# Performance work log

Hardware: AMD Instinct MI355X
Metric: run time of the kernel (lower is better)

The kernel has to match this reference:

```python
import jax, jax.numpy as jnp
import numpy as np

N_NODES = 100000
N_EDGES = 1600000
NFEAT, NHID, NCLASS = 256, 128, 40


def gcn_layer(x, W, b, src, dst, dinv):
    # GCNConv (Kipf): D^-1/2 (A + I) D^-1/2 (X W) + b
    h = x @ W                                    # [N, out]
    coef = (dinv[src] * dinv[dst])[:, None]      # [E, 1] sym-norm per edge
    msg = h[src] * coef                          # gather (irregular access)
    agg = jax.ops.segment_sum(msg, dst, num_segments=N_NODES)
    agg = agg + h * (dinv * dinv)[:, None]       # self-loop contribution
    return agg + b


def setup_inputs() -> dict:
    key = jax.random.key(0)
    ks = jax.random.split(key, 8)
    x = jax.random.normal(ks[0], (N_NODES, NFEAT), dtype=jnp.float32)
    edge_index = jax.random.randint(ks[1], (2, N_EDGES), 0, N_NODES, dtype=jnp.int32)
    def glorot(k, fi, fo):
        s = (6.0 / (fi + fo)) ** 0.5
        return jax.random.uniform(k, (fi, fo), jnp.float32, -s, s)
    return {
        "x": x,
        "edge_index": edge_index,
        "W1": glorot(ks[2], NFEAT, NHID), "b1": jnp.zeros((NHID,), jnp.float32),
        "W2": glorot(ks[3], NHID, NHID), "b2": jnp.zeros((NHID,), jnp.float32),
        "W3": glorot(ks[4], NHID, NCLASS), "b3": jnp.zeros((NCLASS,), jnp.float32),
    }


def reference(x, edge_index, W1, b1, W2, b2, W3, b3):
    src, dst = edge_index[0], edge_index[1]
    # degree with self-loops (count incoming edges per node + 1)
    deg = jax.ops.segment_sum(jnp.ones((N_EDGES,), jnp.float32), dst,
                              num_segments=N_NODES) + 1.0
    dinv = jax.lax.rsqrt(deg)
    h = jax.nn.relu(gcn_layer(x, W1, b1, src, dst, dinv))
    # dropout is identity at eval time
    h = jax.nn.relu(gcn_layer(h, W2, b2, src, dst, dinv))
    h = gcn_layer(h, W3, b3, src, dst, dinv)
    return jax.nn.log_softmax(h, axis=1)
```

## Files before the change

kernel.cpp:

```cpp
#include <hip/hip_runtime.h>
#include <math.h>

#define NFEAT 256
#define NHID 128
#define NCLASS 40
#define BNODES 128
#define BSHIFT 7
#define BCAP 2688
#define MAXBK 1024
#define EPB 16384

typedef unsigned short ushort_t;
typedef unsigned int uint_t;
typedef unsigned char uchar_t;
typedef __attribute__((ext_vector_type(8))) short bf16x8;
typedef __attribute__((ext_vector_type(4))) float f32x4;
typedef __attribute__((ext_vector_type(2))) float f32x2;

static __device__ inline float bf2f(ushort_t u) {
    union { uint_t u; float f; } v; v.u = (uint_t)u << 16; return v.f;
}
static __device__ inline float lo2f(uint_t u) {
    union { uint_t u; float f; } v; v.u = u << 16; return v.f;
}
static __device__ inline float hi2f(uint_t u) {
    union { uint_t u; float f; } v; v.u = u & 0xFFFF0000u; return v.f;
}
static __device__ inline ushort_t f2bf(float f) {
    uint_t u = __float_as_uint(f);
    u += 0x7FFF + ((u >> 16) & 1);
    return (ushort_t)(u >> 16);
}
static __device__ inline float dot2bf(uint_t pk, uint_t mask, float c) {
    float r;
    asm("v_dot2_f32_bf16 %0, %1, %2, %3" : "=v"(r) : "v"(pk), "v"(mask), "v"(c));
    return r;
}
#define LOMASK 0x00003F80u
#define HIMASK 0x3F800000u

static __device__ __forceinline__ void gload16(const void* g, void* l) {
    __builtin_amdgcn_global_load_lds(
        (const __attribute__((address_space(1))) uint_t*)g,
        (__attribute__((address_space(3))) uint_t*)l, 16, 0, 0);
}

static __device__ inline ushort_t pk2fp8(float a, float b) {
    return (ushort_t)__builtin_amdgcn_cvt_pk_fp8_f32(a, b, 0, false);
}
static __device__ inline f32x2 unpk_lo(uint_t w) {
    return __builtin_amdgcn_cvt_pk_f32_fp8(w, false);
}
static __device__ inline f32x2 unpk_hi(uint_t w) {
    return __builtin_amdgcn_cvt_pk_f32_fp8(w, true);
}


__global__ __launch_bounds__(256) void k_ehist(const int* __restrict__ dst,
                                               int* __restrict__ cnt,
                                               int E, int nbk, int nblk) {
    __shared__ int hist[MAXBK];
    int tid = threadIdx.x, be = blockIdx.x;
    for (int i = tid; i < nbk; i += 256) hist[i] = 0;
    __syncthreads();
    int e0 = be * EPB, e1 = min(e0 + EPB, E);
    for (int e = e0 + tid; e < e1; e += 256)
        atomicAdd(&hist[dst[e] >> BSHIFT], 1);
    __syncthreads();
    for (int i = tid; i < nbk; i += 256)
        cnt[(size_t)i * nblk + be] = hist[i];
}

__global__ __launch_bounds__(128) void k_escan(int* __restrict__ cnt,
                                               int* __restrict__ bcnt, int nblk) {
    __shared__ int buf[128];
    int b = blockIdx.x, tid = threadIdx.x;
    int v = (tid < nblk) ? cnt[(size_t)b * nblk + tid] : 0;
    buf[tid] = v;
    __syncthreads();
    for (int off = 1; off < 128; off <<= 1) {
        int t = (tid >= off) ? buf[tid - off] : 0;
        __syncthreads();
        buf[tid] += t;
        __syncthreads();
    }
    if (tid < nblk) cnt[(size_t)b * nblk + tid] = buf[tid] - v;
    if (tid == 127) bcnt[b] = buf[127];
}

__global__ __launch_bounds__(256) void k_escatter(const int* __restrict__ src,
                                                  const int* __restrict__ dst,
                                                  const int* __restrict__ cnt,
                                                  uint_t* __restrict__ bstore,
                                                  int E, int nbk, int nblk) {
    __shared__ int cur[MAXBK];
    int tid = threadIdx.x, be = blockIdx.x;
    for (int i = tid; i < nbk; i += 256)
        cur[i] = cnt[(size_t)i * nblk + be];
    __syncthreads();
    int e0 = be * EPB, e1 = min(e0 + EPB, E);
    for (int e = e0 + tid; e < e1; e += 256) {
        int d = dst[e];
        int b = d >> BSHIFT;
        int p = atomicAdd(&cur[b], 1);
        if (p < BCAP)
            bstore[(size_t)b * BCAP + p] = ((uint_t)(d & (BNODES - 1)) << 20) | (uint_t)src[e];
    }
}


__global__ __launch_bounds__(256) void k_bsort(const uint_t* __restrict__ bstore,
                                               const int* __restrict__ bcnt,
                                               uint_t* __restrict__ colsort,
                                               int* __restrict__ rp,
                                               float* __restrict__ dinv, int N) {
    __shared__ uint_t rec[BCAP];
    __shared__ uint_t srt[BCAP];
    __shared__ int hist[BNODES];
    __shared__ int scan[BNODES];
    __shared__ int cur[BNODES];
    int b = blockIdx.x, tid = threadIdx.x;
    if (tid < BNODES) hist[tid] = 0;
    __syncthreads();
    int cnt = min(bcnt[b], BCAP);
    const uint_t* gp = &bstore[(size_t)b * BCAP];
    for (int e = tid; e < cnt; e += 256) {
        uint_t r = gp[e];
        rec[e] = r;
        atomicAdd(&hist[r >> 20], 1);
    }
    __syncthreads();
    if (tid < BNODES) scan[tid] = hist[tid];
    __syncthreads();
    for (int off = 1; off < BNODES; off <<= 1) {
        int v = 0;
        if (tid < BNODES && tid >= off) v = scan[tid - off];
        __syncthreads();
        if (tid < BNODES) scan[tid] += v;
        __syncthreads();
    }
    if (tid < BNODES) cur[tid] = scan[tid] - hist[tid];
    __syncthreads();
    for (int e = tid; e < cnt; e += 256) {
        uint_t r = rec[e];
        int p = atomicAdd(&cur[r >> 20], 1);
        srt[p] = r & 0xFFFFF;
    }
    __syncthreads();
    uint_t* cs = &colsort[(size_t)b * BCAP];
    for (int e = tid; e < cnt; e += 256) cs[e] = srt[e];
    if (tid < BNODES) {
        rp[b * (BNODES + 1) + tid] = scan[tid] - hist[tid];
        int n = b * BNODES + tid;
        if (n < N) dinv[n] = rsqrtf((float)hist[tid] + 1.0f);
    }
    if (tid == 0) rp[b * (BNODES + 1) + BNODES] = cnt;
}


__global__ __launch_bounds__(256) void k_wtall(const float* __restrict__ W1,
                                               const float* __restrict__ W2,
                                               const float* __restrict__ W3,
                                               ushort_t* __restrict__ T1,
                                               ushort_t* __restrict__ T2,
                                               ushort_t* __restrict__ T3) {
    int idx = blockIdx.x * 256 + threadIdx.x;
    if (idx < NHID * NFEAT) {
        int nrow = idx >> 8, k = idx & 255;
        T1[idx] = f2bf(W1[(size_t)k * NHID + nrow]);
    } else if ((idx -= NHID * NFEAT) < NHID * NHID) {
        int nrow = idx >> 7, kp = idx & 127;
        int s = kp >> 5, pl = kp & 31;
        int k = s * 32 + ((pl & 1) << 4) + (pl >> 1);
        T2[idx] = f2bf(W2[(size_t)k * NHID + nrow]);
    } else if ((idx -= NHID * NHID) < 64 * NHID) {
        int nrow = idx >> 7, kp = idx & 127;
        int s = kp >> 5, pl = kp & 31;
        int k = s * 32 + ((pl & 1) << 4) + (pl >> 1);
        T3[idx] = f2bf(nrow < NCLASS ? W3[(size_t)k * NCLASS + nrow] : 0.f);
    }
}


template<int K, bool A_FP32, int BN, int OST, int MODE>
__global__ __launch_bounds__(512) void k_gemm_mfma(const void* __restrict__ Ap,
                                                   const ushort_t* __restrict__ Whi,
                                                   const float* __restrict__ dinv,
                                                   void* __restrict__ Cv, int n) {
    const int BM = 128, BK = 64;
    __shared__ ushort_t As[BM * BK];
    __shared__ ushort_t Bh[BN * BK];
    const int tid = threadIdx.x;
    const int w = tid >> 6, l = tid & 63;
    const int row0 = blockIdx.x * BM;
    const int NJ = BN / 16;
    f32x4 acc[NJ] = {};

    for (int k0 = 0; k0 < K; k0 += BK) {
        if (A_FP32) {
            int r = tid >> 2;
            if (row0 + r < n) {
                const float* A = (const float*)Ap;
                const float* ap = &A[(size_t)(row0 + r) * K + k0];
#pragma unroll
                for (int h = 0; h < 2; h++) {
                    int q = (tid & 3) * 2 + h;
                    float4 v0 = *(const float4*)&ap[q * 8];
                    float4 v1 = *(const float4*)&ap[q * 8 + 4];
                    ushort4 o0, o1;
                    o0.x = f2bf(v0.x); o0.y = f2bf(v0.y); o0.z = f2bf(v0.z); o0.w = f2bf(v0.w);
                    o1.x = f2bf(v1.x); o1.y = f2bf(v1.y); o1.z = f2bf(v1.z); o1.w = f2bf(v1.w);
                    int pc = q ^ (r & 7);
                    *(ushort4*)&As[r * 64 + pc * 8]     = o0;
                    *(ushort4*)&As[r * 64 + pc * 8 + 4] = o1;
                }
            }
        } else {
            const ushort_t* A = (const ushort_t*)Ap;
#pragma unroll
            for (int m = 0; m < 2; m++) {
                int unit = m * 512 + tid;
                int r = unit >> 3, pc = unit & 7;
                int lc = pc ^ (r & 7);
                int kk = k0 + lc * 8;
                size_t rowg = (size_t)min(row0 + r, n - 1);
                const ushort_t* srcp = &A[(size_t)(kk >> 6) * n * 64 + rowg * 64 + (kk & 63)];
                gload16(srcp, &As[(size_t)unit * 8]);
            }
        }
#pragma unroll
        for (int m = 0; m < BN / 64; m++) {
            int unit = m * 512 + tid;
            int r = unit >> 3, pc = unit & 7;
            int lc = pc ^ (r & 7);
            gload16(&Whi[(size_t)r * K + k0 + lc * 8], &Bh[(size_t)unit * 8]);
        }
        __syncthreads();

        const int lo4 = l & 15;
        const int swz = l & 7;
#pragma unroll
        for (int kh = 0; kh < BK; kh += 32) {
            int q = (kh >> 3) + (l >> 4);
            int ra = w * 16 + lo4;
            bf16x8 a = *(const bf16x8*)&As[ra * 64 + (q ^ swz) * 8];
#pragma unroll
            for (int j = 0; j < NJ; j++) {
                int rb = j * 16 + lo4;
                bf16x8 bh = *(const bf16x8*)&Bh[rb * 64 + (q ^ swz) * 8];
                acc[j] = __builtin_amdgcn_mfma_f32_16x16x32_bf16(a, bh, acc[j], 0, 0, 0);
            }
        }
        __syncthreads();
    }

    float dnv[4];
#pragma unroll
    for (int r = 0; r < 4; r++) {
        int row = row0 + w * 16 + (l >> 4) * 4 + r;
        dnv[r] = (row < n) ? dinv[row] : 0.f;
    }
    const int cb = l & 15;
    if (MODE == 0) {
        uchar_t* C8 = (uchar_t*)Cv;
#pragma unroll
        for (int s = 0; s < NJ / 2; s++) {
            int t = s >> 1, sub = s & 1;
#pragma unroll
            for (int r = 0; r < 4; r++) {
                int row = row0 + w * 16 + (l >> 4) * 4 + r;
                if (row < n) {
                    ushort_t pk = pk2fp8(dnv[r] * acc[2 * s][r], dnv[r] * acc[2 * s + 1][r]);
                    *(ushort_t*)&C8[(size_t)t * n * 64 + (size_t)row * 64 + sub * 32 + cb * 2] = pk;
                }
            }
        }
    } else {
        ushort_t* C = (ushort_t*)Cv;
#pragma unroll
        for (int j = 0; j < NJ; j++) {
#pragma unroll
            for (int r = 0; r < 4; r++) {
                int row = row0 + w * 16 + (l >> 4) * 4 + r;
                if (row < n)
                    C[(size_t)row * OST + j * 16 + cb] = f2bf(dnv[r] * acc[j][r]);
            }
        }
    }
}


__global__ __launch_bounds__(256) void k_agg_slice(const uint_t* __restrict__ colsort,
                                                   const int* __restrict__ rp,
                                                   const uchar_t* __restrict__ h8,
                                                   const float* __restrict__ dinv,
                                                   const float* __restrict__ bias,
                                                   ushort_t* __restrict__ out, int N) {
    __shared__ int srp[BNODES + 1];
    __shared__ uint_t cols[BCAP];
    int blk = blockIdx.x;
    int slice = blk & 1, b = blk >> 1;
    int tid = threadIdx.x;
    if (tid <= BNODES) srp[tid] = rp[b * (BNODES + 1) + tid];
    __syncthreads();
    int cnt = srp[BNODES];
    for (int e = tid; e < cnt; e += 256) cols[e] = colsort[(size_t)b * BCAP + e];
    __syncthreads();
    int fq = tid & 3;
    int q  = tid >> 2;
    const uchar_t* hs = &h8[(size_t)slice * N * 64 + fq * 16];
    float bv[16];
#pragma unroll
    for (int i = 0; i < 16; i++) {
        int p = fq * 16 + i;
        int s = 2 * slice + (p >> 5), pl = p & 31;
        bv[i] = bias[s * 32 + ((pl & 1) << 4) + (pl >> 1)];
    }
    for (int nl = q; nl < BNODES; nl += 64) {
        int n = b * BNODES + nl;
        if (n >= N) break;
        int e = srp[nl], e1 = srp[nl + 1];
        f32x2 a2[8];
        {
            uint4 sv = *(const uint4*)&hs[(size_t)n * 64];
            a2[0] = unpk_lo(sv.x); a2[1] = unpk_hi(sv.x);
            a2[2] = unpk_lo(sv.y); a2[3] = unpk_hi(sv.y);
            a2[4] = unpk_lo(sv.z); a2[5] = unpk_hi(sv.z);
            a2[6] = unpk_lo(sv.w); a2[7] = unpk_hi(sv.w);
        }
        for (; e + 4 <= e1; e += 4) {
            uint4 v[4];
#pragma unroll
            for (int i = 0; i < 4; i++) v[i] = *(const uint4*)&hs[(size_t)cols[e + i] * 64];
#pragma unroll
            for (int i = 0; i < 4; i++) {
                a2[0] += unpk_lo(v[i].x); a2[1] += unpk_hi(v[i].x);
                a2[2] += unpk_lo(v[i].y); a2[3] += unpk_hi(v[i].y);
                a2[4] += unpk_lo(v[i].z); a2[5] += unpk_hi(v[i].z);
                a2[6] += unpk_lo(v[i].w); a2[7] += unpk_hi(v[i].w);
            }
        }
        for (; e < e1; e++) {
            uint4 v = *(const uint4*)&hs[(size_t)cols[e] * 64];
            a2[0] += unpk_lo(v.x); a2[1] += unpk_hi(v.x);
            a2[2] += unpk_lo(v.y); a2[3] += unpk_hi(v.y);
            a2[4] += unpk_lo(v.z); a2[5] += unpk_hi(v.z);
            a2[6] += unpk_lo(v.w); a2[7] += unpk_hi(v.w);
        }
        float dn = dinv[n];
        uint_t o[8];
#pragma unroll
        for (int k = 0; k < 8; k++) {
            float r0 = fmaxf(fmaf(dn, a2[k].x, bv[2 * k]),     0.f);
            float r1 = fmaxf(fmaf(dn, a2[k].y, bv[2 * k + 1]), 0.f);
            o[k] = ((uint_t)f2bf(r1) << 16) | f2bf(r0);
        }
        ushort_t* op = &out[((size_t)slice * N + n) * 64 + fq * 16];
        *(uint4*)&op[0] = make_uint4(o[0], o[1], o[2], o[3]);
        *(uint4*)&op[8] = make_uint4(o[4], o[5], o[6], o[7]);
    }
}


__global__ __launch_bounds__(256) void k_agg40_lsm(const uint_t* __restrict__ colsort,
                                                   const int* __restrict__ rp,
                                                   const ushort_t* __restrict__ h3,
                                                   const float* __restrict__ dinv,
                                                   const float* __restrict__ bias,
                                                   float* __restrict__ out, int N) {
    __shared__ int srp[BNODES + 1];
    __shared__ uint_t cols[BCAP];
    int b = blockIdx.x, tid = threadIdx.x;
    if (tid <= BNODES) srp[tid] = rp[b * (BNODES + 1) + tid];
    __syncthreads();
    int cnt = srp[BNODES];
    for (int e = tid; e < cnt; e += 256) cols[e] = colsort[(size_t)b * BCAP + e];
    __syncthreads();
    int fo = tid & 7;
    int g  = tid >> 3;
    bool act = fo < 5;
    float bv[8];
#pragma unroll
    for (int j = 0; j < 8; j++) bv[j] = act ? bias[fo * 8 + j] : 0.f;
    for (int nl = g; nl < BNODES; nl += 32) {
        int n = b * BNODES + nl;
        if (n >= N) break;
        int e = srp[nl], e1 = srp[nl + 1];
        float a[8] = {0.f, 0.f, 0.f, 0.f, 0.f, 0.f, 0.f, 0.f};
        if (act) {
            uint4 sv = *(const uint4*)&h3[(size_t)n * 64 + fo * 8];
            a[0] = lo2f(sv.x); a[1] = hi2f(sv.x); a[2] = lo2f(sv.y); a[3] = hi2f(sv.y);
            a[4] = lo2f(sv.z); a[5] = hi2f(sv.z); a[6] = lo2f(sv.w); a[7] = hi2f(sv.w);
        }
        for (; e + 4 <= e1; e += 4) {
            if (act) {
                uint4 v[4];
#pragma unroll
                for (int i = 0; i < 4; i++) v[i] = *(const uint4*)&h3[(size_t)cols[e + i] * 64 + fo * 8];
#pragma unroll
                for (int i = 0; i < 4; i++) {
                    a[0] = dot2bf(v[i].x, LOMASK, a[0]); a[1] = dot2bf(v[i].x, HIMASK, a[1]);
                    a[2] = dot2bf(v[i].y, LOMASK, a[2]); a[3] = dot2bf(v[i].y, HIMASK, a[3]);
                    a[4] = dot2bf(v[i].z, LOMASK, a[4]); a[5] = dot2bf(v[i].z, HIMASK, a[5]);
                    a[6] = dot2bf(v[i].w, LOMASK, a[6]); a[7] = dot2bf(v[i].w, HIMASK, a[7]);
                }
            }
        }
        for (; e < e1; e++) {
            if (act) {
                uint4 v = *(const uint4*)&h3[(size_t)cols[e] * 64 + fo * 8];
                a[0] = dot2bf(v.x, LOMASK, a[0]); a[1] = dot2bf(v.x, HIMASK, a[1]);
                a[2] = dot2bf(v.y, LOMASK, a[2]); a[3] = dot2bf(v.y, HIMASK, a[3]);
                a[4] = dot2bf(v.z, LOMASK, a[4]); a[5] = dot2bf(v.z, HIMASK, a[5]);
                a[6] = dot2bf(v.w, LOMASK, a[6]); a[7] = dot2bf(v.w, HIMASK, a[7]);
            }
        }
        float dn = dinv[n];
        float z[8];
        float m = -INFINITY;
#pragma unroll
        for (int j = 0; j < 8; j++) {
            z[j] = act ? fmaf(dn, a[j], bv[j]) : -INFINITY;
            m = fmaxf(m, z[j]);
        }
#pragma unroll
        for (int off = 4; off; off >>= 1) m = fmaxf(m, __shfl_xor(m, off, 8));
        float p = 0.f;
        if (act) {
#pragma unroll
            for (int j = 0; j < 8; j++) p += expf(z[j] - m);
        }
#pragma unroll
        for (int off = 4; off; off >>= 1) p += __shfl_xor(p, off, 8);
        float lse = m + logf(p);
        if (act) {
            float4 o0 = make_float4(z[0] - lse, z[1] - lse, z[2] - lse, z[3] - lse);
            float4 o1 = make_float4(z[4] - lse, z[5] - lse, z[6] - lse, z[7] - lse);
            *(float4*)&out[(size_t)n * NCLASS + fo * 8]     = o0;
            *(float4*)&out[(size_t)n * NCLASS + fo * 8 + 4] = o1;
        }
    }
}


extern "C" void kernel_launch(void* const* d_in, const int* in_sizes, int n_in,
                              void* d_out, int out_size, void* d_ws, size_t ws_size,
                              hipStream_t stream) {
    const float* x  = (const float*)d_in[0];
    const int*   ei = (const int*)d_in[1];
    const float* W1 = (const float*)d_in[2];
    const float* b1 = (const float*)d_in[3];
    const float* W2 = (const float*)d_in[4];
    const float* b2 = (const float*)d_in[5];
    const float* W3 = (const float*)d_in[6];
    const float* b3 = (const float*)d_in[7];
    float* out = (float*)d_out;
    const int N = in_sizes[0] / NFEAT;
    const int E = in_sizes[1] / 2;
    const int* src = ei;
    const int* dst = ei + E;
    const int NBK = (N + BNODES - 1) / BNODES;
    const int NBLK_E = (E + EPB - 1) / EPB;

    char* ws = (char*)d_ws;
    size_t off = 0;
    auto alloc = [&](size_t bytes) -> void* {
        void* p = ws + off;
        off += (bytes + 255) & ~(size_t)255;
        return p;
    };
    int*      bcnt    = (int*)alloc((size_t)NBK * 4);
    int*      ecnt    = (int*)alloc((size_t)NBK * NBLK_E * 4);
    uint_t*   bstore  = (uint_t*)alloc((size_t)NBK * BCAP * 4);
    uint_t*   colsort = (uint_t*)alloc((size_t)NBK * BCAP * 4);
    int*      rp      = (int*)alloc((size_t)NBK * (BNODES + 1) * 4);
    float*    dinv    = (float*)alloc((size_t)N * 4);
    uchar_t*  h8      = (uchar_t*)alloc((size_t)N * NHID);
    ushort_t* abuf    = (ushort_t*)alloc((size_t)N * NHID * 2);
    ushort_t* h3      = (ushort_t*)alloc((size_t)N * 64 * 2);
    ushort_t* Whi1    = (ushort_t*)alloc((size_t)NHID * NFEAT * 2);
    ushort_t* Whi2    = (ushort_t*)alloc((size_t)NHID * NHID * 2);
    ushort_t* Whi3    = (ushort_t*)alloc((size_t)64 * NHID * 2);
    (void)ws_size; (void)n_in; (void)out_size;

    int wtelems = NHID * NFEAT + NHID * NHID + 64 * NHID;
    k_wtall<<<(wtelems + 255) / 256, 256, 0, stream>>>(W1, W2, W3, Whi1, Whi2, Whi3);

    k_ehist<<<NBLK_E, 256, 0, stream>>>(dst, ecnt, E, NBK, NBLK_E);
    k_escan<<<NBK, 128, 0, stream>>>(ecnt, bcnt, NBLK_E);
    k_escatter<<<NBLK_E, 256, 0, stream>>>(src, dst, ecnt, bstore, E, NBK, NBLK_E);
    k_bsort<<<NBK, 256, 0, stream>>>(bstore, bcnt, colsort, rp, dinv, N);

    int ngemm = (N + 127) / 128;
    k_gemm_mfma<NFEAT, true, 128, 0, 0><<<ngemm, 512, 0, stream>>>(x, Whi1, dinv, h8, N);
    k_agg_slice<<<NBK * 2, 256, 0, stream>>>(colsort, rp, h8, dinv, b1, abuf, N);
    k_gemm_mfma<NHID, false, 128, 0, 0><<<ngemm, 512, 0, stream>>>(abuf, Whi2, dinv, h8, N);
    k_agg_slice<<<NBK * 2, 256, 0, stream>>>(colsort, rp, h8, dinv, b2, abuf, N);
    k_gemm_mfma<NHID, false, 64, 64, 1><<<ngemm, 512, 0, stream>>>(abuf, Whi3, dinv, h3, N);
    k_agg40_lsm<<<NBK, 256, 0, stream>>>(colsort, rp, h3, dinv, b3, out, N);
}
```

Measured before the change: 238.4 us.

## Locally sort edges by bucket in LDS before coalesced scatter to global

The edge scatter kernel now builds a per-block histogram and prefix scan, sorts its edges by destination bucket in shared memory, and then writes them to the global bucket store in contiguous runs instead of issuing random scattered writes. Edges per block are halved so the sorted chunk fits in LDS, and the count scan is widened to 256 threads to cover the doubled number of edge blocks. The aim is to coalesce the global writes, at the cost of a redundant histogram pass, extra LDS traffic, more blocks, and large LDS use per block that can limit occupancy.

```diff
diff --git a/kernel.cpp b/kernel.cpp
--- a/kernel.cpp
+++ b/kernel.cpp
@@ -8,7 +8,7 @@
 #define BSHIFT 7
 #define BCAP 2688
 #define MAXBK 1024
-#define EPB 16384
+#define EPB 8192
 
 typedef unsigned short ushort_t;
 typedef unsigned int uint_t;
@@ -71,21 +71,21 @@
         cnt[(size_t)i * nblk + be] = hist[i];
 }
 
-__global__ __launch_bounds__(128) void k_escan(int* __restrict__ cnt,
+__global__ __launch_bounds__(256) void k_escan(int* __restrict__ cnt,
                                                int* __restrict__ bcnt, int nblk) {
-    __shared__ int buf[128];
+    __shared__ int buf[256];
     int b = blockIdx.x, tid = threadIdx.x;
     int v = (tid < nblk) ? cnt[(size_t)b * nblk + tid] : 0;
     buf[tid] = v;
     __syncthreads();
-    for (int off = 1; off < 128; off <<= 1) {
+    for (int off = 1; off < 256; off <<= 1) {
         int t = (tid >= off) ? buf[tid - off] : 0;
         __syncthreads();
         buf[tid] += t;
         __syncthreads();
     }
     if (tid < nblk) cnt[(size_t)b * nblk + tid] = buf[tid] - v;
-    if (tid == 127) bcnt[b] = buf[127];
+    if (tid == 255) bcnt[b] = buf[255];
 }
 
 __global__ __launch_bounds__(256) void k_escatter(const int* __restrict__ src,
@@ -93,18 +93,53 @@
                                                   const int* __restrict__ cnt,
                                                   uint_t* __restrict__ bstore,
                                                   int E, int nbk, int nblk) {
-    __shared__ int cur[MAXBK];
+    __shared__ uint_t   sorted[EPB];
+    __shared__ ushort_t sortb[EPB];
+    __shared__ int hist[MAXBK];
+    __shared__ int lcur[MAXBK];
+    __shared__ int gadj[MAXBK];
+    __shared__ int buf[256];
     int tid = threadIdx.x, be = blockIdx.x;
-    for (int i = tid; i < nbk; i += 256)
-        cur[i] = cnt[(size_t)i * nblk + be];
+    for (int i = tid; i < MAXBK; i += 256) hist[i] = 0;
     __syncthreads();
     int e0 = be * EPB, e1 = min(e0 + EPB, E);
+    for (int e = e0 + tid; e < e1; e += 256)
+        atomicAdd(&hist[dst[e] >> BSHIFT], 1);
+    __syncthreads();
+    int base = tid * 4;
+    int v0 = hist[base], v1 = hist[base + 1], v2 = hist[base + 2], v3 = hist[base + 3];
+    int s = v0 + v1 + v2 + v3;
+    buf[tid] = s;
+    __syncthreads();
+    for (int off = 1; off < 256; off <<= 1) {
+        int t = (tid >= off) ? buf[tid - off] : 0;
+        __syncthreads();
+        buf[tid] += t;
+        __syncthreads();
+    }
+    int run = buf[tid] - s;
+    int ls0 = run, ls1 = run + v0, ls2 = run + v0 + v1, ls3 = run + v0 + v1 + v2;
+    gadj[base]     = ((base     < nbk) ? cnt[(size_t)(base)     * nblk + be] : 0) - ls0;
+    gadj[base + 1] = ((base + 1 < nbk) ? cnt[(size_t)(base + 1) * nblk + be] : 0) - ls1;
+    gadj[base + 2] = ((base + 2 < nbk) ? cnt[(size_t)(base + 2) * nblk + be] : 0) - ls2;
+    gadj[base + 3] = ((base + 3 < nbk) ? cnt[(size_t)(base + 3) * nblk + be] : 0) - ls3;
+    lcur[base] = ls0; lcur[base + 1] = ls1; lcur[base + 2] = ls2; lcur[base + 3] = ls3;
+    __syncthreads();
     for (int e = e0 + tid; e < e1; e += 256) {
         int d = dst[e];
         int b = d >> BSHIFT;
-        int p = atomicAdd(&cur[b], 1);
-        if (p < BCAP)
-            bstore[(size_t)b * BCAP + p] = ((uint_t)(d & (BNODES - 1)) << 20) | (uint_t)src[e];
+        uint_t rec = ((uint_t)(d & (BNODES - 1)) << 20) | (uint_t)src[e];
+        int p = atomicAdd(&lcur[b], 1);
+        sorted[p] = rec;
+        sortb[p] = (ushort_t)b;
+    }
+    __syncthreads();
+    int cntL = e1 - e0;
+    for (int i = tid; i < cntL; i += 256) {
+        int bb = sortb[i];
+        int idx = gadj[bb] + i;
+        if (idx < BCAP)
+            bstore[(size_t)bb * BCAP + idx] = sorted[i];
     }
 }
 
@@ -487,7 +522,7 @@
     k_wtall<<<(wtelems + 255) / 256, 256, 0, stream>>>(W1, W2, W3, Whi1, Whi2, Whi3);
 
     k_ehist<<<NBLK_E, 256, 0, stream>>>(dst, ecnt, E, NBK, NBLK_E);
-    k_escan<<<NBK, 128, 0, stream>>>(ecnt, bcnt, NBLK_E);
+    k_escan<<<NBK, 256, 0, stream>>>(ecnt, bcnt, NBLK_E);
     k_escatter<<<NBLK_E, 256, 0, stream>>>(src, dst, ecnt, bstore, E, NBK, NBLK_E);
     k_bsort<<<NBK, 256, 0, stream>>>(bstore, bcnt, colsort, rp, dinv, N);
 
```

After: 212.7 us. 10.8% less time.
